# Optimization experiments

Hardware: AMD Instinct MI355X
Metric: run time of the kernel (lower is better)

## Reference

```python
import jax, jax.numpy as jnp
import numpy as np

H = 8          # num query heads
KV = 1         # num kv heads
D = 256        # head_dim
HID = 2048     # hidden_size
B = 4          # sequences in prefill batch
S = 2048       # tokens per sequence
T = B * S      # total tokens
NUM_SLOTS = 16384
ROPE_THETA = 10000.0


def setup_inputs() -> dict:
    key = jax.random.key(0)
    k1, k2, k3 = jax.random.split(key, 3)
    hidden_states = jax.random.normal(k1, (T, HID), dtype=jnp.float32)
    # real rotary tables: positions 0..S-1 repeated per sequence
    pos = jnp.tile(jnp.arange(S, dtype=jnp.float32), B)              # [T]
    inv_freq = 1.0 / (ROPE_THETA ** (jnp.arange(0, D, 2, dtype=jnp.float32) / D))  # [D/2]
    ang = pos[:, None] * inv_freq[None, :]                            # [T, D/2]
    cos, sin = jnp.cos(ang), jnp.sin(ang)
    slots = jnp.arange(T, dtype=jnp.int32)                            # contiguous slot mapping
    key_cache = jnp.zeros((NUM_SLOTS, KV, D), dtype=jnp.float32)
    value_cache = jnp.zeros((NUM_SLOTS, KV, D), dtype=jnp.float32)
    w_qkv = jax.random.normal(k2, ((H + 2 * KV) * D, HID), dtype=jnp.float32) * (HID ** -0.5)
    w_o = jax.random.normal(k3, (HID, H * D), dtype=jnp.float32) * ((H * D) ** -0.5)
    return {"hidden_states": hidden_states, "cos": cos, "sin": sin, "slots": slots,
            "key_cache": key_cache, "value_cache": value_cache, "w_qkv": w_qkv, "w_o": w_o}


def _rope(x, cos, sin):
    # rotate-half convention: x:[T, h, D], cos/sin:[T, D/2]
    x1, x2 = x[..., : D // 2], x[..., D // 2 :]
    c, s = cos[:, None, :], sin[:, None, :]
    return jnp.concatenate([x1 * c - x2 * s, x2 * c + x1 * s], axis=-1)


def reference(hidden_states, cos, sin, slots, key_cache, value_cache, w_qkv, w_o):
    qkv = hidden_states @ w_qkv.T                                  # [T, (H+2KV)*D]
    q = qkv[:, : H * D].reshape(T, H, D)
    k = qkv[:, H * D : (H + KV) * D].reshape(T, KV, D)
    v = qkv[:, (H + KV) * D :].reshape(T, KV, D)
    q = _rope(q, cos, sin)
    k = _rope(k, cos, sin)
    # paged_attention.reshape_and_cache: scatter post-RoPE k and raw v into cache slots
    key_cache = key_cache.at[slots].set(k)
    value_cache = value_cache.at[slots].set(v)
    # prefill flash attention: causal, per-sequence (equal-length ragged batch)
    qb = q.reshape(B, S, H, D)
    kb = jnp.repeat(k.reshape(B, S, KV, D), H // KV, axis=2)       # GQA expand
    vb = jnp.repeat(v.reshape(B, S, KV, D), H // KV, axis=2)
    scale = D ** -0.5
    scores = jnp.einsum("bqhd,bkhd->bhqk", qb, kb) * scale          # [B,H,S,S]
    causal = jnp.tril(jnp.ones((S, S), dtype=bool))
    scores = jnp.where(causal[None, None], scores, jnp.finfo(scores.dtype).min)
    probs = jax.nn.softmax(scores, axis=-1)
    attn = jnp.einsum("bhqk,bkhd->bqhd", probs, vb).reshape(T, H * D)
    out = attn @ w_o.T                                              # [T, HID]
    return out, key_cache, value_cache
```

## Files before the change

kernel.cpp:

```cpp
#include <hip/hip_runtime.h>

#define HN 8
#define DH 256
#define HID 2048
#define BB 4
#define SS 2048
#define TT (BB*SS)
#define NQKV 2560
#define NSLOTS 16384

typedef unsigned short u16;
typedef unsigned int u32;
typedef __bf16 bf16x8 __attribute__((ext_vector_type(8)));
typedef float f32x4 __attribute__((ext_vector_type(4)));
typedef u16 u16x4 __attribute__((ext_vector_type(4)));
typedef u16 u16x8 __attribute__((ext_vector_type(8)));

__device__ __forceinline__ u16 f2bf(float f) {
    u32 u = __builtin_bit_cast(u32, f);
    u = u + 0x7fffu + ((u >> 16) & 1u);
    return (u16)(u >> 16);
}
__device__ __forceinline__ float bf2f(u16 h) {
    u32 u = ((u32)h) << 16;
    return __builtin_bit_cast(float, u);
}
__device__ __forceinline__ void gload_lds16(const void* g, void* l) {
    __builtin_amdgcn_global_load_lds((__attribute__((address_space(1))) void*)g,
                                     (__attribute__((address_space(3))) void*)l,
                                     16, 0, 0);
}
__device__ __forceinline__ u32 cvtpk_bf16(float a, float b) {
    u32 r;
    asm("v_cvt_pk_bf16_f32 %0, %1, %2" : "=v"(r) : "v"(a), "v"(b));
    return r;
}

__global__ __launch_bounds__(256) void cvt_f32_bf16(const float* __restrict__ in,
                                                    u16* __restrict__ out, long n) {
    long i = ((long)blockIdx.x * blockDim.x + threadIdx.x) * 4;
    long stride = (long)gridDim.x * blockDim.x * 4;
    for (; i < n; i += stride) {
        float4 v = *(const float4*)(in + i);
        u16x4 o4;
        o4[0] = f2bf(v.x); o4[1] = f2bf(v.y); o4[2] = f2bf(v.z); o4[3] = f2bf(v.w);
        *(u16x4*)(out + i) = o4;
    }
}

template<int OUTBF>
__global__ __launch_bounds__(256) void gemm_nt(const u16* __restrict__ A, const u16* __restrict__ B,
                                               void* __restrict__ C, int M, int N, int K) {
    __shared__ u16 As[128 * 32];
    __shared__ u16 Bs[128 * 32];
    const int tid = threadIdx.x;
    const int lane = tid & 63, w = tid >> 6;
    const int quad = lane >> 4, m16 = lane & 15;
    const int wm = w & 1, wn = w >> 1;
    const int r4 = tid >> 2, c8 = (tid & 3) * 8;
    const long arow = (long)blockIdx.x * 128;
    const long brow = (long)blockIdx.y * 128;

    f32x4 acc[4][4];
#pragma unroll
    for (int i = 0; i < 4; i++)
#pragma unroll
        for (int j = 0; j < 4; j++) acc[i][j] = (f32x4){0.f, 0.f, 0.f, 0.f};

    const u16* Ag = A + (arow + r4) * (long)K + c8;
    const u16* Bg = B + (brow + r4) * (long)K + c8;

    for (int k0 = 0; k0 < K; k0 += 32) {
        __syncthreads();
        gload_lds16(Ag + k0,                 (char*)As + tid * 16);
        gload_lds16(Ag + 64l * K + k0,       (char*)As + 4096 + tid * 16);
        gload_lds16(Bg + k0,                 (char*)Bs + tid * 16);
        gload_lds16(Bg + 64l * K + k0,       (char*)Bs + 4096 + tid * 16);
        __syncthreads();
        bf16x8 af[4], bfr[4];
#pragma unroll
        for (int mi = 0; mi < 4; mi++)
            af[mi] = *(const bf16x8*)(As + (wm * 64 + mi * 16 + m16) * 32 + quad * 8);
#pragma unroll
        for (int ni = 0; ni < 4; ni++)
            bfr[ni] = *(const bf16x8*)(Bs + (wn * 64 + ni * 16 + m16) * 32 + quad * 8);
#pragma unroll
        for (int mi = 0; mi < 4; mi++)
#pragma unroll
            for (int ni = 0; ni < 4; ni++)
                acc[mi][ni] = __builtin_amdgcn_mfma_f32_16x16x32_bf16(af[mi], bfr[ni], acc[mi][ni], 0, 0, 0);
    }
#pragma unroll
    for (int mi = 0; mi < 4; mi++) {
#pragma unroll
        for (int ni = 0; ni < 4; ni++) {
            long col = brow + wn * 64 + ni * 16 + m16;
#pragma unroll
            for (int r = 0; r < 4; r++) {
                long row = arow + wm * 64 + mi * 16 + quad * 4 + r;
                float v = acc[mi][ni][r];
                if (OUTBF) ((u16*)C)[row * N + col] = f2bf(v);
                else       ((float*)C)[row * N + col] = v;
            }
        }
    }
}

__global__ __launch_bounds__(256) void rope_scatter(u16* __restrict__ qkv, const float* __restrict__ cosb,
        const float* __restrict__ sinb, const int* __restrict__ slots,
        u16* __restrict__ kb, float* __restrict__ kc, float* __restrict__ vc) {
    const int t = blockIdx.x, tid = threadIdx.x;
    const long qbase = (long)t * NQKV;
#pragma unroll
    for (int i = 0; i < 4; i++) {
        int idx = tid + i * 256;
        int head = idx >> 7, d = idx & 127;
        long off = qbase + head * DH + d;
        float q1 = bf2f(qkv[off]), q2 = bf2f(qkv[off + 128]);
        float c = cosb[(long)t * 128 + d], s = sinb[(long)t * 128 + d];
        qkv[off]       = f2bf((q1 * c - q2 * s) * 0.0625f);
        qkv[off + 128] = f2bf((q2 * c + q1 * s) * 0.0625f);
    }
    const int slot = slots[t];
    if (tid < 128) {
        int d = tid;
        long off = qbase + HN * DH + d;
        float k1 = bf2f(qkv[off]), k2 = bf2f(qkv[off + 128]);
        float c = cosb[(long)t * 128 + d], s = sinb[(long)t * 128 + d];
        float kn1 = k1 * c - k2 * s, kn2 = k2 * c + k1 * s;
        kb[(long)t * DH + d]       = f2bf(kn1);
        kb[(long)t * DH + d + 128] = f2bf(kn2);
        kc[(long)slot * DH + d]       = kn1;
        kc[(long)slot * DH + d + 128] = kn2;
    }
    {
        int d = tid;
        vc[(long)slot * DH + d] = bf2f(qkv[qbase + (HN + 1) * DH + d]);
    }
}

__global__ __launch_bounds__(256) void transpose_v(const u16* __restrict__ qkv, u16* __restrict__ vbt) {
    const int tid = threadIdx.x;
    const int s0 = blockIdx.x * 64, d0 = blockIdx.y * 64, b = blockIdx.z;
#pragma unroll
    for (int i = 0; i < 2; i++) {
        int d = d0 + i * 32 + (tid >> 3);
        int s = s0 + (tid & 7) * 8;
        u16x8 v;
#pragma unroll
        for (int e = 0; e < 8; e++)
            v[e] = qkv[(long)(b * SS + s + e) * NQKV + (HN + 1) * DH + d];
        *(u16x8*)(vbt + ((long)b * DH + d) * SS + s) = v;
    }
}

__global__ __launch_bounds__(256, 4) void flash_attn(const u16* __restrict__ qkv, const u16* __restrict__ kb,
                                                     const u16* __restrict__ vbt, u16* __restrict__ attn) {
    __shared__ u16 Ks[32 * 256];
    __shared__ u16 Vt[256 * 32];
    const int tid = threadIdx.x;
    const int lane = tid & 63, w = tid >> 6;
    const int quad = lane >> 4, m16 = lane & 15;
    const int xr = blockIdx.x & 7, xt = blockIdx.x >> 3;
    const int qb = (xt == 0) ? 31 - xr : (xt == 1) ? 16 + xr : (xt == 2) ? 15 - xr : xr;
    const int h = blockIdx.y, b = blockIdx.z;
    const int qrow_w = qb * 64 + w * 16;

    const int krow = tid >> 5, kg = tid & 31, kgs = kg ^ krow;
    const int ks_hi = (krow >> 2) << 3, ks_lo = krow & 3;
    const int vrow = tid >> 2, vg = tid & 3,  vgs = vg ^ ((vrow >> 1) & 3);
    const int km7 = m16 & 7;
    const int vcol = (quad ^ ((m16 >> 1) & 3)) * 8;

    bf16x8 aq[8];
    {
        const u16* qp = qkv + (long)(b * SS + qrow_w + m16) * NQKV + h * DH;
#pragma unroll
        for (int ks = 0; ks < 8; ks++)
            aq[ks] = *(const bf16x8*)(qp + ks * 32 + quad * 8);
    }
    f32x4 o[16];
#pragma unroll
    for (int i = 0; i < 16; i++) o[i] = (f32x4){0.f, 0.f, 0.f, 0.f};
    float m_run = -1e30f;
    float l_run = 0.f;
    const long kvrow0 = (long)b * SS;
    const u16* vbase = vbt + (long)b * DH * SS;
    const int ntiles = 2 * qb + 2;

    for (int it = 0; it < ntiles; it++) {
        const int kv0 = it * 32;
        __syncthreads();
#pragma unroll
        for (int i = 0; i < 4; i++) {
            const int srcrow = ((i & 1) << 4) + ks_hi + ((i >> 1) << 2) + ks_lo;
            gload_lds16(kb + (kvrow0 + kv0 + srcrow) * DH + kgs * 8,
                        (char*)Ks + i * 4096 + tid * 16);
            gload_lds16(vbase + (long)(i * 64 + vrow) * SS + kv0 + vgs * 8,
                        (char*)Vt + i * 4096 + tid * 16);
        }
        asm volatile("s_waitcnt vmcnt(0)" ::: "memory");
        __syncthreads();

        if (kv0 <= qrow_w + 15) {
            f32x4 sc[2];
            sc[0] = (f32x4){0.f, 0.f, 0.f, 0.f};
            sc[1] = (f32x4){0.f, 0.f, 0.f, 0.f};
            __builtin_amdgcn_s_setprio(1);
#pragma unroll
            for (int ks = 0; ks < 8; ks++)
#pragma unroll
                for (int n = 0; n < 2; n++) {
                    bf16x8 kf = *(const bf16x8*)(Ks + (n * 16 + m16) * 256 + (((ks * 4 + quad) ^ km7) << 3));
                    sc[n] = __builtin_amdgcn_mfma_f32_16x16x32_bf16(kf, aq[ks], sc[n], 0, 0, 0);
                }
            __builtin_amdgcn_s_setprio(0);
            if (kv0 >= qb * 64) {
                const int qg = qrow_w + m16;
                const int kvb = kv0 + quad * 8;
#pragma unroll
                for (int n = 0; n < 2; n++)
#pragma unroll
                    for (int r = 0; r < 4; r++)
                        if (kvb + n * 4 + r > qg) sc[n][r] = -1e30f;
            }
            float mx = fmaxf(fmaxf(fmaxf(sc[0][0], sc[0][1]), fmaxf(sc[0][2], sc[0][3])),
                             fmaxf(fmaxf(sc[1][0], sc[1][1]), fmaxf(sc[1][2], sc[1][3])));
            if (__any((int)(mx > m_run + 8.f))) {
                float mr = fmaxf(mx, __shfl_xor(mx, 16));
                mr = fmaxf(mr, __shfl_xor(mr, 32));
                float mn = fmaxf(m_run, mr);
                float alpha = __expf(m_run - mn);
                m_run = mn;
                l_run *= alpha;
                float ar[4];
#pragma unroll
                for (int r = 0; r < 4; r++) ar[r] = __shfl(alpha, quad * 4 + r);
#pragma unroll
                for (int nf = 0; nf < 16; nf++)
#pragma unroll
                    for (int r = 0; r < 4; r++) o[nf][r] *= ar[r];
            }
#pragma unroll
            for (int n = 0; n < 2; n++)
#pragma unroll
                for (int r = 0; r < 4; r++) {
                    float p = __expf(sc[n][r] - m_run);
                    sc[n][r] = p;
                    l_run += p;
                }
            union { u32 w4[4]; bf16x8 v; } pu;
            pu.w4[0] = cvtpk_bf16(sc[0][0], sc[0][1]);
            pu.w4[1] = cvtpk_bf16(sc[0][2], sc[0][3]);
            pu.w4[2] = cvtpk_bf16(sc[1][0], sc[1][1]);
            pu.w4[3] = cvtpk_bf16(sc[1][2], sc[1][3]);
            __builtin_amdgcn_s_setprio(1);
#pragma unroll
            for (int nf = 0; nf < 16; nf++) {
                bf16x8 vf = *(const bf16x8*)(Vt + (nf * 16 + m16) * 32 + vcol);
                o[nf] = __builtin_amdgcn_mfma_f32_16x16x32_bf16(pu.v, vf, o[nf], 0, 0, 0);
            }
            __builtin_amdgcn_s_setprio(0);
        }
    }
    l_run += __shfl_xor(l_run, 16);
    l_run += __shfl_xor(l_run, 32);
    float invm = 1.f / l_run;
    float ir[4];
#pragma unroll
    for (int r = 0; r < 4; r++) ir[r] = __shfl(invm, quad * 4 + r);
#pragma unroll
    for (int nf = 0; nf < 16; nf++)
#pragma unroll
        for (int r = 0; r < 4; r++) {
            long row = (long)(b * SS + qrow_w + quad * 4 + r);
            attn[row * (HN * DH) + h * DH + nf * 16 + m16] = f2bf(o[nf][r] * ir[r]);
        }
}

extern "C" void kernel_launch(void* const* d_in, const int* in_sizes, int n_in,
                              void* d_out, int out_size, void* d_ws, size_t ws_size,
                              hipStream_t stream) {
    (void)in_sizes; (void)n_in; (void)out_size; (void)ws_size;
    const float* hidden = (const float*)d_in[0];
    const float* cosb   = (const float*)d_in[1];
    const float* sinb   = (const float*)d_in[2];
    const int*   slots  = (const int*)d_in[3];
    const float* kc_in  = (const float*)d_in[4];
    const float* vc_in  = (const float*)d_in[5];
    const float* w_qkv  = (const float*)d_in[6];
    const float* w_o    = (const float*)d_in[7];

    float* out    = (float*)d_out;
    float* kc_out = out + (size_t)TT * HID;
    float* vc_out = kc_out + (size_t)NSLOTS * DH;

    char* p = (char*)d_ws;
    u16* hid_b  = (u16*)p;  p += (size_t)TT * HID * 2;
    u16* wqkv_b = (u16*)p;  p += (size_t)NQKV * HID * 2;
    u16* wo_b   = (u16*)p;  p += (size_t)HID * HID * 2;
    u16* kb     = (u16*)p;  p += (size_t)TT * DH * 2;
    u16* vbt    = (u16*)p;  p += (size_t)TT * DH * 2;
    u16* attn_b = hid_b;
    u16* qkv_b  = (u16*)d_out;

    hipMemcpyAsync(kc_out, kc_in, (size_t)NSLOTS * DH * 4, hipMemcpyDeviceToDevice, stream);
    hipMemcpyAsync(vc_out, vc_in, (size_t)NSLOTS * DH * 4, hipMemcpyDeviceToDevice, stream);

    cvt_f32_bf16<<<dim3(2048), dim3(256), 0, stream>>>(hidden, hid_b, (long)TT * HID);
    cvt_f32_bf16<<<dim3(640),  dim3(256), 0, stream>>>(w_qkv, wqkv_b, (long)NQKV * HID);
    cvt_f32_bf16<<<dim3(512),  dim3(256), 0, stream>>>(w_o,   wo_b,   (long)HID * HID);

    gemm_nt<1><<<dim3(TT / 128, NQKV / 128), dim3(256), 0, stream>>>(hid_b, wqkv_b, qkv_b, TT, NQKV, HID);
    rope_scatter<<<dim3(TT), dim3(256), 0, stream>>>(qkv_b, cosb, sinb, slots, kb, kc_out, vc_out);
    transpose_v<<<dim3(SS / 64, DH / 64, BB), dim3(256), 0, stream>>>(qkv_b, vbt);
    flash_attn<<<dim3(SS / 64, HN, BB), dim3(256), 0, stream>>>(qkv_b, kb, vbt, attn_b);
    gemm_nt<0><<<dim3(TT / 128, HID / 128), dim3(256), 0, stream>>>(attn_b, wo_b, out, TT, HID, HID);
}
```

Measured before the change: 646.4 us.

## Load V fragments directly from global, LDS-tile V transpose, reorder attention blocks

The V tile is no longer staged in shared memory. Each lane now reads its bf16x8 V fragment straight from the transposed V buffer in global memory/L2, which halves LDS use per block and allows launch bounds to rise to 6 blocks per CU. The V transpose kernel now goes through an LDS tile, so its global reads and writes are coalesced. The attention grid is flattened across batches with a heavy-to-light causal ordering for load balance. The cost is uncoalesced-ish global loads inside the inner MFMA loop, which adds latency per tile.

```diff
diff --git a/kernel.cpp b/kernel.cpp
--- a/kernel.cpp
+++ b/kernel.cpp
@@ -140,37 +140,42 @@
 }
 
 __global__ __launch_bounds__(256) void transpose_v(const u16* __restrict__ qkv, u16* __restrict__ vbt) {
+    __shared__ u16 Ls[64][66];
     const int tid = threadIdx.x;
     const int s0 = blockIdx.x * 64, d0 = blockIdx.y * 64, b = blockIdx.z;
+    const int lr = tid >> 3, lc = (tid & 7) * 8;
 #pragma unroll
     for (int i = 0; i < 2; i++) {
-        int d = d0 + i * 32 + (tid >> 3);
-        int s = s0 + (tid & 7) * 8;
+        int s = s0 + i * 32 + lr;
+        u16x8 v = *(const u16x8*)(qkv + (long)(b * SS + s) * NQKV + (HN + 1) * DH + d0 + lc);
+        *(u16x8*)(&Ls[i * 32 + lr][lc]) = v;
+    }
+    __syncthreads();
+#pragma unroll
+    for (int i = 0; i < 2; i++) {
+        int d = i * 32 + lr;
         u16x8 v;
 #pragma unroll
-        for (int e = 0; e < 8; e++)
-            v[e] = qkv[(long)(b * SS + s + e) * NQKV + (HN + 1) * DH + d];
-        *(u16x8*)(vbt + ((long)b * DH + d) * SS + s) = v;
-    }
-}
-
-__global__ __launch_bounds__(256, 4) void flash_attn(const u16* __restrict__ qkv, const u16* __restrict__ kb,
+        for (int e = 0; e < 8; e++) v[e] = Ls[lc + e][d];
+        *(u16x8*)(vbt + ((long)b * DH + d0 + d) * SS + s0 + lc) = v;
+    }
+}
+
+__global__ __launch_bounds__(256, 6) void flash_attn(const u16* __restrict__ qkv, const u16* __restrict__ kb,
                                                      const u16* __restrict__ vbt, u16* __restrict__ attn) {
     __shared__ u16 Ks[32 * 256];
-    __shared__ u16 Vt[256 * 32];
     const int tid = threadIdx.x;
     const int lane = tid & 63, w = tid >> 6;
     const int quad = lane >> 4, m16 = lane & 15;
-    const int xr = blockIdx.x & 7, xt = blockIdx.x >> 3;
-    const int qb = (xt == 0) ? 31 - xr : (xt == 1) ? 16 + xr : (xt == 2) ? 15 - xr : xr;
-    const int h = blockIdx.y, b = blockIdx.z;
+    const int xr = blockIdx.x & 7, t = blockIdx.x >> 3;
+    const int s_cls = xr & 1, b = xr >> 1;
+    const int qb = (t < 8) ? (31 - 2 * t - s_cls) : (2 * (t - 8) + s_cls);
+    const int h = blockIdx.y;
     const int qrow_w = qb * 64 + w * 16;
 
     const int krow = tid >> 5, kg = tid & 31, kgs = kg ^ krow;
     const int ks_hi = (krow >> 2) << 3, ks_lo = krow & 3;
-    const int vrow = tid >> 2, vg = tid & 3,  vgs = vg ^ ((vrow >> 1) & 3);
     const int km7 = m16 & 7;
-    const int vcol = (quad ^ ((m16 >> 1) & 3)) * 8;
 
     bf16x8 aq[8];
     {
@@ -185,7 +190,7 @@
     float m_run = -1e30f;
     float l_run = 0.f;
     const long kvrow0 = (long)b * SS;
-    const u16* vbase = vbt + (long)b * DH * SS;
+    const u16* vlane = vbt + ((long)b * DH + m16) * SS + quad * 8;
     const int ntiles = 2 * qb + 2;
 
     for (int it = 0; it < ntiles; it++) {
@@ -196,8 +201,6 @@
             const int srcrow = ((i & 1) << 4) + ks_hi + ((i >> 1) << 2) + ks_lo;
             gload_lds16(kb + (kvrow0 + kv0 + srcrow) * DH + kgs * 8,
                         (char*)Ks + i * 4096 + tid * 16);
-            gload_lds16(vbase + (long)(i * 64 + vrow) * SS + kv0 + vgs * 8,
-                        (char*)Vt + i * 4096 + tid * 16);
         }
         asm volatile("s_waitcnt vmcnt(0)" ::: "memory");
         __syncthreads();
@@ -254,10 +257,11 @@
             pu.w4[1] = cvtpk_bf16(sc[0][2], sc[0][3]);
             pu.w4[2] = cvtpk_bf16(sc[1][0], sc[1][1]);
             pu.w4[3] = cvtpk_bf16(sc[1][2], sc[1][3]);
+            const u16* vt = vlane + kv0;
             __builtin_amdgcn_s_setprio(1);
 #pragma unroll
             for (int nf = 0; nf < 16; nf++) {
-                bf16x8 vf = *(const bf16x8*)(Vt + (nf * 16 + m16) * 32 + vcol);
+                bf16x8 vf = *(const bf16x8*)(vt + (long)nf * 16 * SS);
                 o[nf] = __builtin_amdgcn_mfma_f32_16x16x32_bf16(pu.v, vf, o[nf], 0, 0, 0);
             }
             __builtin_amdgcn_s_setprio(0);
@@ -314,6 +318,6 @@
     gemm_nt<1><<<dim3(TT / 128, NQKV / 128), dim3(256), 0, stream>>>(hid_b, wqkv_b, qkv_b, TT, NQKV, HID);
     rope_scatter<<<dim3(TT), dim3(256), 0, stream>>>(qkv_b, cosb, sinb, slots, kb, kc_out, vc_out);
     transpose_v<<<dim3(SS / 64, DH / 64, BB), dim3(256), 0, stream>>>(qkv_b, vbt);
-    flash_attn<<<dim3(SS / 64, HN, BB), dim3(256), 0, stream>>>(qkv_b, kb, vbt, attn_b);
+    flash_attn<<<dim3(4 * 32, HN, 1), dim3(256), 0, stream>>>(qkv_b, kb, vbt, attn_b);
     gemm_nt<0><<<dim3(TT / 128, HID / 128), dim3(256), 0, stream>>>(attn_b, wo_b, out, TT, HID, HID);
 }
```

Result: slower. 1.345 ms (+108.0%).
